# Optimization experiments

Measured on AMD Instinct MI355X. Metric: run time of the kernel, lower is better.

Reference implementation:

```python
import jax, jax.numpy as jnp
import numpy as np

DEG = 2
KNOTS = (0.25, 0.5, 0.75)
CONDITION_DIM = 1
INPUT_DIM = 1024
OUTPUT_DIM = 1024
NUM_BASIS = DEG + 1 + len(KNOTS)  # 6
BATCH = 32768


def setup_inputs() -> dict:
    key = jax.random.key(0)
    k1, k2, k3 = jax.random.split(key, 3)
    # x carries [features | condition] concatenated along dim 1
    x = jax.random.uniform(k1, (BATCH, INPUT_DIM + CONDITION_DIM), dtype=jnp.float32)
    fan_in = INPUT_DIM  # kaiming-style scale for the weight tensor
    weight = jax.random.normal(k2, (NUM_BASIS * CONDITION_DIM, INPUT_DIM, OUTPUT_DIM), dtype=jnp.float32) / np.sqrt(fan_in)
    bias_param = jax.random.normal(k3, (OUTPUT_DIM,), dtype=jnp.float32) / np.sqrt(fan_in)
    return {"x": x, "weight": weight, "bias_param": bias_param}


def _basis(condition):
    # condition: (B, condition_dim). Truncated power spline basis per condition column.
    cols = []
    for j in range(CONDITION_DIM):
        t = condition[:, j]
        for i in range(DEG + 1):
            cols.append(t ** i)
        for knot in KNOTS:
            cols.append(jax.nn.relu(t - knot) ** DEG)
    return jnp.stack(cols, axis=1)  # (B, coef_dim)


def reference(x, weight, bias_param):
    feats = x[:, :INPUT_DIM]            # (B, d)
    condition = x[:, INPUT_DIM:]        # (B, condition_dim)
    basis = _basis(condition)           # (B, c)
    # Same math as einsum('bc,cde->bde') then ('bde,bd->be'), but contracted in
    # the cheaper order (avoids the (B, d, e) per-sample weight tensor):
    xw = jnp.einsum('bd,cde->bce', feats, weight)   # (B, c, e)
    out = jnp.einsum('bc,bce->be', basis, xw)       # (B, e)
    return out + bias_param
```

## Files before the change

### kernel.cpp

```cpp
#include <hip/hip_runtime.h>
#include <stdint.h>

#define IN_DIM    1024
#define OUT_DIM   1024
#define ROWSTRIDE 1025
#define BATCH     32768
#define NBASIS    6
#define KTOT      (NBASIS * IN_DIM)
#define KSTEPS    96

typedef __bf16 bf16x8 __attribute__((ext_vector_type(8)));
typedef float  f32x4  __attribute__((ext_vector_type(4)));

__device__ inline unsigned short f2bf(float f) {
  union { float f; unsigned u; } v; v.f = f;
  unsigned u = v.u;
  return (unsigned short)((u + 0x7FFFu + ((u >> 16) & 1u)) >> 16);
}

__global__ __launch_bounds__(256) void prep_f(const float* __restrict__ x,
                                              unsigned short* __restrict__ F,
                                              float* __restrict__ bas_t) {
  const int tid = threadIdx.x;
  const int rl  = tid >> 7;
  const int j   = tid & 127;
  for (int rb = blockIdx.x * 2 + rl; rb < BATCH; rb += 4096) {
    const float* xr = x + (size_t)rb * ROWSTRIDE;
    unsigned short* fr = F + (size_t)rb * IN_DIM;
    #pragma unroll
    for (int i = 0; i < 4; ++i) {
      float v0 = xr[2 * j + 256 * i];
      float v1 = xr[2 * j + 1 + 256 * i];
      unsigned pw = (unsigned)f2bf(v0) | ((unsigned)f2bf(v1) << 16);
      *(unsigned*)(fr + 2 * j + 256 * i) = pw;
    }
    if (j == 0) {
      float t  = xr[IN_DIM];
      float r1 = fmaxf(t - 0.25f, 0.0f);
      float r2 = fmaxf(t - 0.50f, 0.0f);
      float r3 = fmaxf(t - 0.75f, 0.0f);
      bas_t[rb]             = 1.0f;
      bas_t[BATCH + rb]     = t;
      bas_t[2 * BATCH + rb] = t * t;
      bas_t[3 * BATCH + rb] = r1 * r1;
      bas_t[4 * BATCH + rb] = r2 * r2;
      bas_t[5 * BATCH + rb] = r3 * r3;
    }
  }
}

__global__ void prep_wt(const float* __restrict__ w, unsigned short* __restrict__ bt) {
  __shared__ unsigned short t[32][33];
  int k0 = blockIdx.x * 32;
  int e0 = blockIdx.y * 32;
  int tid = threadIdx.x;
  #pragma unroll
  for (int p = tid; p < 1024; p += 256) {
    int kk = p >> 5, ee = p & 31;
    t[ee][kk] = f2bf(w[(size_t)(k0 + kk) * OUT_DIM + e0 + ee]);
  }
  __syncthreads();
  #pragma unroll
  for (int p = tid; p < 1024; p += 256) {
    int ee = p >> 5, kk = p & 31;
    bt[(size_t)(e0 + ee) * KTOT + k0 + kk] = t[ee][kk];
  }
}

__device__ inline void gload_lds16(const unsigned short* g, unsigned short* l) {
  __builtin_amdgcn_global_load_lds((const __attribute__((address_space(1))) void*)g,
                                   (__attribute__((address_space(3))) void*)l, 16, 0, 0);
}

__device__ __attribute__((always_inline)) inline
void scale_store(uint4 w, float s, unsigned short* dst) {
  bf16x8 r;
  unsigned q0 = w.x, q1 = w.y, q2 = w.z, q3 = w.w;
  r[0] = (__bf16)(__uint_as_float(q0 << 16) * s);
  r[1] = (__bf16)(__uint_as_float(q0 & 0xFFFF0000u) * s);
  r[2] = (__bf16)(__uint_as_float(q1 << 16) * s);
  r[3] = (__bf16)(__uint_as_float(q1 & 0xFFFF0000u) * s);
  r[4] = (__bf16)(__uint_as_float(q2 << 16) * s);
  r[5] = (__bf16)(__uint_as_float(q2 & 0xFFFF0000u) * s);
  r[6] = (__bf16)(__uint_as_float(q3 << 16) * s);
  r[7] = (__bf16)(__uint_as_float(q3 & 0xFFFF0000u) * s);
  *(bf16x8*)dst = r;
}

template<int I0>
__device__ __attribute__((always_inline)) inline
void cluster(f32x4 (&acc)[8][4], const bf16x8* afr, const bf16x8* bfr) {
  __builtin_amdgcn_s_setprio(1);
  #pragma unroll
  for (int i = 0; i < 4; ++i) {
    #pragma unroll
    for (int j = 0; j < 4; ++j)
      acc[I0 + i][j] =
          __builtin_amdgcn_mfma_f32_16x16x32_bf16(afr[i], bfr[j], acc[I0 + i][j], 0, 0, 0);
  }
  __builtin_amdgcn_s_setprio(0);
}

__global__ __launch_bounds__(512, 2) void vcl_gemm(
    const unsigned short* __restrict__ F,
    const unsigned short* __restrict__ BT,
    const float* __restrict__ bas_t,
    const float* __restrict__ bias,
    float* __restrict__ out) {
  __shared__ __align__(16) unsigned short smem[65536];
  unsigned short* const sA0 = smem;
  unsigned short* const sA1 = smem + 16384;
  unsigned short* const sB0 = smem + 32768;
  unsigned short* const sB1 = smem + 49152;

  const int tid  = threadIdx.x;
  const int wv   = tid >> 6;
  const int lane = tid & 63;
  const int ln15 = lane & 15;
  const int quad = lane >> 4;
  const int lr   = lane >> 3;
  const int kg   = lane & 7;
  const int wm   = wv >> 2;
  const int wn   = wv & 3;

  const int bm0 = (blockIdx.x >> 2) * 256;
  const int bn0 = (blockIdx.x & 3) * 256;

  int arow[4]; unsigned agoff[4]; int awoff[4];
  const unsigned short* gB[4]; int lboff[4];
  #pragma unroll
  for (int w = 0; w < 4; ++w) {
    arow[w]  = wv * 32 + w * 8 + lr;
    agoff[w] = (unsigned)(bm0 + arow[w]) * 1024u + (unsigned)(kg * 8);
    awoff[w] = arow[w] * 128 + ((kg ^ lr) << 4);
    gB[w]    = BT + (size_t)(bn0 + arow[w]) * KTOT + (kg ^ lr) * 8;
    lboff[w] = (wv * 4 + w) * 512;
  }

  const int slot0 = quad ^ (ln15 & 7);
  const int aoff0 = (wm * 128 + ln15) * 64 + slot0 * 8;
  const int boff0 = (wn * 64 + ln15) * 64 + slot0 * 8;

  float bias_j[4];
  #pragma unroll
  for (int jj = 0; jj < 4; ++jj) bias_j[jj] = bias[bn0 + wn * 64 + jj * 16 + ln15];

  float s_[4];
  #pragma unroll
  for (int w = 0; w < 4; ++w) s_[w] = bas_t[bm0 + arow[w]];

  f32x4 acc[8][4] = {};

  {
    uint4 ad0[4];
    #pragma unroll
    for (int w = 0; w < 4; ++w) ad0[w] = *(const uint4*)(F + agoff[w]);
    #pragma unroll
    for (int w = 0; w < 4; ++w) gload_lds16(gB[w], sB0 + lboff[w]);
    #pragma unroll
    for (int w = 0; w < 4; ++w)
      scale_store(ad0[w], s_[w], (unsigned short*)((char*)sA0 + awoff[w]));
    asm volatile("s_waitcnt lgkmcnt(0)" ::: "memory");
  }

  for (int t = 0; t < KSTEPS; ++t) {
    const unsigned short* sAc = (t & 1) ? sA1 : sA0;
    const unsigned short* sBc = (t & 1) ? sB1 : sB0;
    unsigned short* sAn = (t & 1) ? sA0 : sA1;
    unsigned short* sBn = (t & 1) ? sB0 : sB1;
    const int tn = (t + 1 == KSTEPS) ? 0 : (t + 1);
    const int doffA = (tn & 15) * 64;
    const unsigned offB = (unsigned)(tn * 64);

    if ((tn & 15) == 0) {
      const int c = tn >> 4;
      #pragma unroll
      for (int w = 0; w < 4; ++w)
        s_[w] = bas_t[(size_t)c * BATCH + bm0 + arow[w]];
    }
    uint4 ad[4];
    #pragma unroll
    for (int w = 0; w < 4; ++w) ad[w] = *(const uint4*)(F + agoff[w] + doffA);
    #pragma unroll
    for (int w = 0; w < 4; ++w) gload_lds16(gB[w] + offB, sBn + lboff[w]);

    asm volatile("s_waitcnt vmcnt(8)" ::: "memory");
    __builtin_amdgcn_s_barrier();
    __builtin_amdgcn_sched_barrier(0);

    bf16x8 afr[4], bfr[4];

    #pragma unroll
    for (int j = 0; j < 4; ++j) bfr[j] = *(const bf16x8*)(sBc + boff0 + j * 1024);
    #pragma unroll
    for (int i = 0; i < 4; ++i) afr[i] = *(const bf16x8*)(sAc + aoff0 + i * 1024);
    cluster<0>(acc, afr, bfr);

    #pragma unroll
    for (int i = 0; i < 4; ++i) afr[i] = *(const bf16x8*)(sAc + aoff0 + (i + 4) * 1024);
    cluster<4>(acc, afr, bfr);

    scale_store(ad[0], s_[0], (unsigned short*)((char*)sAn + awoff[0]));
    scale_store(ad[1], s_[1], (unsigned short*)((char*)sAn + awoff[1]));
    scale_store(ad[2], s_[2], (unsigned short*)((char*)sAn + awoff[2]));
    scale_store(ad[3], s_[3], (unsigned short*)((char*)sAn + awoff[3]));

    #pragma unroll
    for (int j = 0; j < 4; ++j) bfr[j] = *(const bf16x8*)(sBc + (boff0 ^ 32) + j * 1024);
    #pragma unroll
    for (int i = 0; i < 4; ++i) afr[i] = *(const bf16x8*)(sAc + (aoff0 ^ 32) + i * 1024);
    cluster<0>(acc, afr, bfr);

    #pragma unroll
    for (int i = 0; i < 4; ++i) afr[i] = *(const bf16x8*)(sAc + (aoff0 ^ 32) + (i + 4) * 1024);
    cluster<4>(acc, afr, bfr);

    asm volatile("s_waitcnt lgkmcnt(0)" ::: "memory");
    __builtin_amdgcn_sched_barrier(0);
    __builtin_amdgcn_s_barrier();
    __builtin_amdgcn_sched_barrier(0);
  }

  float* buf = (float*)smem;
  const int ROWP = 260;
  const int erow = tid >> 3;
  const int echk = tid & 7;

  #pragma unroll
  for (int g = 0; g < 4; ++g) {
    __syncthreads();
    if (wm == (g >> 1)) {
      const int i0 = (g & 1) * 4;
      #pragma unroll
      for (int ii = 0; ii < 4; ++ii) {
        #pragma unroll
        for (int j = 0; j < 4; ++j) {
          #pragma unroll
          for (int r = 0; r < 4; ++r)
            buf[(ii * 16 + quad * 4 + r) * ROWP + wn * 64 + j * 16 + ln15] =
                acc[i0 + ii][j][r] + bias_j[j];
        }
      }
    }
    __syncthreads();
    float* orow = out + (size_t)(bm0 + g * 64 + erow) * OUT_DIM + bn0 + echk * 32;
    const float* brow = buf + erow * ROWP + echk * 32;
    #pragma unroll
    for (int e = 0; e < 8; ++e)
      *(f32x4*)(orow + e * 4) = *(const f32x4*)(brow + e * 4);
  }
}

extern "C" void kernel_launch(void* const* d_in, const int* in_sizes, int n_in,
                              void* d_out, int out_size, void* d_ws, size_t ws_size,
                              hipStream_t stream) {
  const float* x    = (const float*)d_in[0];
  const float* w    = (const float*)d_in[1];
  const float* bias = (const float*)d_in[2];
  float* out = (float*)d_out;

  unsigned short* F  = (unsigned short*)d_ws;
  unsigned short* BT = (unsigned short*)((char*)d_ws + (size_t)BATCH * IN_DIM * 2);
  float* bas_t = (float*)((char*)d_ws + (size_t)BATCH * IN_DIM * 2 + (size_t)OUT_DIM * KTOT * 2);

  prep_f<<<2048, 256, 0, stream>>>(x, F, bas_t);
  dim3 g2(KTOT / 32, OUT_DIM / 32);
  prep_wt<<<g2, 256, 0, stream>>>(w, BT);
  vcl_gemm<<<(BATCH / 256) * (OUT_DIM / 256), 512, 0, stream>>>(F, BT, bas_t, bias, out);
}
```

Measured before the change: 706.3 us.

## Reorder K loop to reuse loaded feature tile across all six basis scalings

The K loop is restructured from 96 flat steps into 16 feature chunks times 6 basis coefficients. Each global F fragment is now loaded once and reused, scaled by six different basis values, instead of being reloaded for every basis. Basis scalars are staged into LDS up front, and the scale_store calls are interleaved between MFMA clusters. The B operand is reindexed to match the new order. This cuts global/L2 traffic for F and removes per-step global loads, at the cost of a fully unrolled six-step body with more code and registers, and vmcnt waits that vary per step.

After: 691.7 us. 1.02x faster.

```diff
diff --git a/kernel.cpp b/kernel.cpp
--- a/kernel.cpp
+++ b/kernel.cpp
@@ -7,7 +7,6 @@
 #define BATCH     32768
 #define NBASIS    6
 #define KTOT      (NBASIS * IN_DIM)
-#define KSTEPS    96
 
 typedef __bf16 bf16x8 __attribute__((ext_vector_type(8)));
 typedef float  f32x4  __attribute__((ext_vector_type(4)));
@@ -101,6 +100,61 @@
   __builtin_amdgcn_s_setprio(0);
 }
 
+#define KSTEP(CC, WSTR)                                                                    \
+  {                                                                                        \
+    const unsigned short* sAc = ((CC) & 1) ? sA1 : sA0;                                    \
+    const unsigned short* sBc = ((CC) & 1) ? sB1 : sB0;                                    \
+    unsigned short* sAn = ((CC) & 1) ? sA0 : sA1;                                          \
+    unsigned short* sBn = ((CC) & 1) ? sB0 : sB1;                                          \
+    const unsigned offB = ((CC) < 5) ? (unsigned)((((CC) + 1) << 10) | (d << 6))           \
+                                     : (unsigned)(dn1 << 6);                               \
+    gload_lds16(BT + gBoff[0] + offB, sBn + lboff[0]);                                     \
+    gload_lds16(BT + gBoff[1] + offB, sBn + lboff[1]);                                     \
+    gload_lds16(BT + gBoff[2] + offB, sBn + lboff[2]);                                     \
+    gload_lds16(BT + gBoff[3] + offB, sBn + lboff[3]);                                     \
+    if ((CC) == 0) {                                                                       \
+      adn[0] = *(const uint4*)(F + agoff[0] + (dn1 << 6));                                 \
+      adn[1] = *(const uint4*)(F + agoff[1] + (dn1 << 6));                                 \
+      adn[2] = *(const uint4*)(F + agoff[2] + (dn1 << 6));                                 \
+      adn[3] = *(const uint4*)(F + agoff[3] + (dn1 << 6));                                 \
+    }                                                                                      \
+    asm volatile("s_waitcnt " WSTR ::: "memory");                                          \
+    __builtin_amdgcn_s_barrier();                                                          \
+    __builtin_amdgcn_sched_barrier(0);                                                     \
+    const int ci_ = ((CC) < 5) ? (CC) + 1 : 0;                                             \
+    float sc0 = bas_lds[ci_ * 256 + arow[0]];                                              \
+    float sc1 = bas_lds[ci_ * 256 + arow[1]];                                              \
+    float sc2 = bas_lds[ci_ * 256 + arow[2]];                                              \
+    float sc3 = bas_lds[ci_ * 256 + arow[3]];                                              \
+    const uint4* asrc = ((CC) < 5) ? ad : adn;                                             \
+    bf16x8 afr[4], bfr[4];                                                                 \
+    _Pragma("unroll")                                                                      \
+    for (int j = 0; j < 4; ++j) bfr[j] = *(const bf16x8*)(sBc + boff0 + j * 1024);         \
+    _Pragma("unroll")                                                                      \
+    for (int i = 0; i < 4; ++i) afr[i] = *(const bf16x8*)(sAc + aoff0 + i * 1024);         \
+    cluster<0>(acc, afr, bfr);                                                             \
+    scale_store(asrc[0], sc0, (unsigned short*)((char*)sAn + awoff[0]));                   \
+    _Pragma("unroll")                                                                      \
+    for (int i = 0; i < 4; ++i) afr[i] = *(const bf16x8*)(sAc + aoff0 + (i + 4) * 1024);   \
+    cluster<4>(acc, afr, bfr);                                                             \
+    scale_store(asrc[1], sc1, (unsigned short*)((char*)sAn + awoff[1]));                   \
+    _Pragma("unroll")                                                                      \
+    for (int j = 0; j < 4; ++j) bfr[j] = *(const bf16x8*)(sBc + (boff0 ^ 32) + j * 1024);  \
+    _Pragma("unroll")                                                                      \
+    for (int i = 0; i < 4; ++i) afr[i] = *(const bf16x8*)(sAc + (aoff0 ^ 32) + i * 1024);  \
+    cluster<0>(acc, afr, bfr);                                                             \
+    scale_store(asrc[2], sc2, (unsigned short*)((char*)sAn + awoff[2]));                   \
+    _Pragma("unroll")                                                                      \
+    for (int i = 0; i < 4; ++i)                                                            \
+      afr[i] = *(const bf16x8*)(sAc + (aoff0 ^ 32) + (i + 4) * 1024);                      \
+    cluster<4>(acc, afr, bfr);                                                             \
+    scale_store(asrc[3], sc3, (unsigned short*)((char*)sAn + awoff[3]));                   \
+    asm volatile("s_waitcnt lgkmcnt(0)" ::: "memory");                                     \
+    __builtin_amdgcn_sched_barrier(0);                                                     \
+    __builtin_amdgcn_s_barrier();                                                          \
+    __builtin_amdgcn_sched_barrier(0);                                                     \
+  }
+
 __global__ __launch_bounds__(512, 2) void vcl_gemm(
     const unsigned short* __restrict__ F,
     const unsigned short* __restrict__ BT,
@@ -108,6 +162,7 @@
     const float* __restrict__ bias,
     float* __restrict__ out) {
   __shared__ __align__(16) unsigned short smem[65536];
+  __shared__ __align__(16) float bas_lds[NBASIS * 256];
   unsigned short* const sA0 = smem;
   unsigned short* const sA1 = smem + 16384;
   unsigned short* const sB0 = smem + 32768;
@@ -127,13 +182,13 @@
   const int bn0 = (blockIdx.x & 3) * 256;
 
   int arow[4]; unsigned agoff[4]; int awoff[4];
-  const unsigned short* gB[4]; int lboff[4];
+  unsigned gBoff[4]; int lboff[4];
   #pragma unroll
   for (int w = 0; w < 4; ++w) {
     arow[w]  = wv * 32 + w * 8 + lr;
     agoff[w] = (unsigned)(bm0 + arow[w]) * 1024u + (unsigned)(kg * 8);
     awoff[w] = arow[w] * 128 + ((kg ^ lr) << 4);
-    gB[w]    = BT + (size_t)(bn0 + arow[w]) * KTOT + (kg ^ lr) * 8;
+    gBoff[w] = (unsigned)(bn0 + arow[w]) * (unsigned)KTOT + (unsigned)((kg ^ lr) * 8);
     lboff[w] = (wv * 4 + w) * 512;
   }
 
@@ -141,85 +196,41 @@
   const int aoff0 = (wm * 128 + ln15) * 64 + slot0 * 8;
   const int boff0 = (wn * 64 + ln15) * 64 + slot0 * 8;
 
+  for (int p = tid; p < NBASIS * 256; p += 512)
+    bas_lds[p] = bas_t[(size_t)(p >> 8) * BATCH + bm0 + (p & 255)];
+  __syncthreads();
+
+  f32x4 acc[8][4] = {};
+  uint4 ad[4], adn[4];
+
+  #pragma unroll
+  for (int w = 0; w < 4; ++w) ad[w] = *(const uint4*)(F + agoff[w]);
+  #pragma unroll
+  for (int w = 0; w < 4; ++w) gload_lds16(BT + gBoff[w], sB0 + lboff[w]);
+  {
+    float s0 = bas_lds[arow[0]], s1 = bas_lds[arow[1]];
+    float s2 = bas_lds[arow[2]], s3 = bas_lds[arow[3]];
+    scale_store(ad[0], s0, (unsigned short*)((char*)sA0 + awoff[0]));
+    scale_store(ad[1], s1, (unsigned short*)((char*)sA0 + awoff[1]));
+    scale_store(ad[2], s2, (unsigned short*)((char*)sA0 + awoff[2]));
+    scale_store(ad[3], s3, (unsigned short*)((char*)sA0 + awoff[3]));
+  }
+  asm volatile("s_waitcnt lgkmcnt(0)" ::: "memory");
+
+  for (int d = 0; d < 16; ++d) {
+    const int dn1 = (d + 1) & 15;
+    KSTEP(0, "vmcnt(8)")
+    KSTEP(1, "vmcnt(8)")
+    KSTEP(2, "vmcnt(4)")
+    KSTEP(3, "vmcnt(4)")
+    KSTEP(4, "vmcnt(4)")
+    KSTEP(5, "vmcnt(4)")
+    ad[0] = adn[0]; ad[1] = adn[1]; ad[2] = adn[2]; ad[3] = adn[3];
+  }
+
   float bias_j[4];
   #pragma unroll
   for (int jj = 0; jj < 4; ++jj) bias_j[jj] = bias[bn0 + wn * 64 + jj * 16 + ln15];
-
-  float s_[4];
-  #pragma unroll
-  for (int w = 0; w < 4; ++w) s_[w] = bas_t[bm0 + arow[w]];
-
-  f32x4 acc[8][4] = {};
-
-  {
-    uint4 ad0[4];
-    #pragma unroll
-    for (int w = 0; w < 4; ++w) ad0[w] = *(const uint4*)(F + agoff[w]);
-    #pragma unroll
-    for (int w = 0; w < 4; ++w) gload_lds16(gB[w], sB0 + lboff[w]);
-    #pragma unroll
-    for (int w = 0; w < 4; ++w)
-      scale_store(ad0[w], s_[w], (unsigned short*)((char*)sA0 + awoff[w]));
-    asm volatile("s_waitcnt lgkmcnt(0)" ::: "memory");
-  }
-
-  for (int t = 0; t < KSTEPS; ++t) {
-    const unsigned short* sAc = (t & 1) ? sA1 : sA0;
-    const unsigned short* sBc = (t & 1) ? sB1 : sB0;
-    unsigned short* sAn = (t & 1) ? sA0 : sA1;
-    unsigned short* sBn = (t & 1) ? sB0 : sB1;
-    const int tn = (t + 1 == KSTEPS) ? 0 : (t + 1);
-    const int doffA = (tn & 15) * 64;
-    const unsigned offB = (unsigned)(tn * 64);
-
-    if ((tn & 15) == 0) {
-      const int c = tn >> 4;
-      #pragma unroll
-      for (int w = 0; w < 4; ++w)
-        s_[w] = bas_t[(size_t)c * BATCH + bm0 + arow[w]];
-    }
-    uint4 ad[4];
-    #pragma unroll
-    for (int w = 0; w < 4; ++w) ad[w] = *(const uint4*)(F + agoff[w] + doffA);
-    #pragma unroll
-    for (int w = 0; w < 4; ++w) gload_lds16(gB[w] + offB, sBn + lboff[w]);
-
-    asm volatile("s_waitcnt vmcnt(8)" ::: "memory");
-    __builtin_amdgcn_s_barrier();
-    __builtin_amdgcn_sched_barrier(0);
-
-    bf16x8 afr[4], bfr[4];
-
-    #pragma unroll
-    for (int j = 0; j < 4; ++j) bfr[j] = *(const bf16x8*)(sBc + boff0 + j * 1024);
-    #pragma unroll
-    for (int i = 0; i < 4; ++i) afr[i] = *(const bf16x8*)(sAc + aoff0 + i * 1024);
-    cluster<0>(acc, afr, bfr);
-
-    #pragma unroll
-    for (int i = 0; i < 4; ++i) afr[i] = *(const bf16x8*)(sAc + aoff0 + (i + 4) * 1024);
-    cluster<4>(acc, afr, bfr);
-
-    scale_store(ad[0], s_[0], (unsigned short*)((char*)sAn + awoff[0]));
-    scale_store(ad[1], s_[1], (unsigned short*)((char*)sAn + awoff[1]));
-    scale_store(ad[2], s_[2], (unsigned short*)((char*)sAn + awoff[2]));
-    scale_store(ad[3], s_[3], (unsigned short*)((char*)sAn + awoff[3]));
-
-    #pragma unroll
-    for (int j = 0; j < 4; ++j) bfr[j] = *(const bf16x8*)(sBc + (boff0 ^ 32) + j * 1024);
-    #pragma unroll
-    for (int i = 0; i < 4; ++i) afr[i] = *(const bf16x8*)(sAc + (aoff0 ^ 32) + i * 1024);
-    cluster<0>(acc, afr, bfr);
-
-    #pragma unroll
-    for (int i = 0; i < 4; ++i) afr[i] = *(const bf16x8*)(sAc + (aoff0 ^ 32) + (i + 4) * 1024);
-    cluster<4>(acc, afr, bfr);
-
-    asm volatile("s_waitcnt lgkmcnt(0)" ::: "memory");
-    __builtin_amdgcn_sched_barrier(0);
-    __builtin_amdgcn_s_barrier();
-    __builtin_amdgcn_sched_barrier(0);
-  }
 
   float* buf = (float*)smem;
   const int ROWP = 260;
```
